# Kernel tuning notes

Measured on AMD Instinct MI355X. Metric: run time of the kernel, lower is better.

Reference implementation:

```python
import jax, jax.numpy as jnp
import numpy as np

NUM_NODES = 100000
NUM_EDGES = 2500000
NUM_GRAPHS = 512
IN_DIM = 14
HID = 32
N_EXTRA_CONVS = 4  # num_layers - 1


def setup_inputs() -> dict:
    key = jax.random.key(0)
    ks = jax.random.split(key, 16)
    x = jax.random.normal(ks[0], (NUM_NODES, IN_DIM), dtype=jnp.float32)
    edge_index = jax.random.randint(ks[1], (2, NUM_EDGES), 0, NUM_NODES, dtype=jnp.int64)
    batch = jnp.sort(jax.random.randint(ks[2], (NUM_NODES,), 0, NUM_GRAPHS, dtype=jnp.int64))
    s = 1.0 / np.sqrt(HID)
    # PyG GraphConv: out = lin_rel(aggr_add(x_j)) + lin_root(x_i); lin_rel has bias, lin_root has no bias
    W_rel1 = jax.random.uniform(ks[3], (IN_DIM, HID), jnp.float32, -s, s)
    b_rel1 = jax.random.uniform(ks[4], (HID,), jnp.float32, -s, s)
    W_root1 = jax.random.uniform(ks[5], (IN_DIM, HID), jnp.float32, -s, s)
    W_rel = jax.random.uniform(ks[6], (N_EXTRA_CONVS, HID, HID), jnp.float32, -s, s)
    b_rel = jax.random.uniform(ks[7], (N_EXTRA_CONVS, HID), jnp.float32, -s, s)
    W_root = jax.random.uniform(ks[8], (N_EXTRA_CONVS, HID, HID), jnp.float32, -s, s)
    lin1_w = jax.random.uniform(ks[9], (HID, HID), jnp.float32, -s, s)
    lin1_b = jax.random.uniform(ks[10], (HID,), jnp.float32, -s, s)
    lin2_w = jax.random.uniform(ks[11], (HID, 2), jnp.float32, -s, s)
    lin2_b = jax.random.uniform(ks[12], (2,), jnp.float32, -s, s)
    return {
        "x": x, "W_rel1": W_rel1, "b_rel1": b_rel1, "W_root1": W_root1,
        "W_rel": W_rel, "b_rel": b_rel, "W_root": W_root,
        "lin1_w": lin1_w, "lin1_b": lin1_b, "lin2_w": lin2_w, "lin2_b": lin2_b,
        "edge_index": edge_index, "batch": batch,
    }


def reference(x, W_rel1, b_rel1, W_root1, W_rel, b_rel, W_root,
              lin1_w, lin1_b, lin2_w, lin2_b, edge_index, batch):
    src, dst = edge_index[0], edge_index[1]

    def graph_conv(h, wr, br, wroot):
        # sum-aggregate neighbor features: scatter-add messages h[src] into dst
        agg = jax.ops.segment_sum(h[src], dst, num_segments=NUM_NODES)
        return agg @ wr + br + h @ wroot

    h = jax.nn.relu(graph_conv(x, W_rel1, b_rel1, W_root1))
    for i in range(N_EXTRA_CONVS):
        h = jax.nn.relu(graph_conv(h, W_rel[i], b_rel[i], W_root[i]))
    # sum pooling per graph
    g = jax.ops.segment_sum(h, batch, num_segments=NUM_GRAPHS)
    g = jax.nn.relu(g @ lin1_w + lin1_b)
    # dropout is identity in eval mode
    logits = g @ lin2_w + lin2_b
    return jax.nn.log_softmax(logits, axis=1)
```

## Files before the change

### kernel.cpp

```cpp
#include <hip/hip_runtime.h>
#include <math.h>

#define N_NODES 100000
#define N_EDGES 2500000
#define N_GRAPHS 512
#define IN_DIM 14
#define HID 32
#define CAP 64

#define BSHIFT 7
#define BNODES 128
#define NB 782
#define NBP 784
#define NBANKS 8
#define SUBCAP 512
#define BCAP 4096
#define CHUNK 4096
#define TB_BIN 512
#define NBLK_E ((N_EDGES + CHUNK - 1) / CHUNK)
#define EPT (CHUNK / TB_BIN)

#define GSTRIDE 8
#define GCUR_N (NBP * NBANKS * GSTRIDE)

typedef unsigned int uint;
typedef unsigned short ushort;
typedef float v2f __attribute__((ext_vector_type(2)));

__device__ inline float bflo(uint w) { return __uint_as_float(w << 16); }
__device__ inline float bfhi(uint w) { return __uint_as_float(w & 0xffff0000u); }
__device__ inline ushort f2bf(float f) {
    uint u = __float_as_uint(f);
    return (ushort)((u + 0x7fffu + ((u >> 16) & 1u)) >> 16);
}

__global__ void bin_edges(const int* __restrict__ src, const int* __restrict__ dst,
                          int* __restrict__ gcur, int* __restrict__ binned) {
    __shared__ int scnt[NBP];
    __shared__ int sbase[NBP];
    int t = threadIdx.x;
    for (int i = t; i < NBP; i += TB_BIN) scnt[i] = 0;
    __syncthreads();
    int base = blockIdx.x * CHUNK;
    int bank = blockIdx.x & (NBANKS - 1);
    int dreg[EPT];
    int rreg[EPT];
#pragma unroll
    for (int j = 0; j < EPT; ++j) {
        int e = base + j * TB_BIN + t;
        dreg[j] = (e < N_EDGES) ? __builtin_nontemporal_load(dst + e) : -1;
        rreg[j] = (dreg[j] >= 0) ? atomicAdd(&scnt[dreg[j] >> BSHIFT], 1) : 0;
    }
    __syncthreads();
    for (int b = t; b < NBP; b += TB_BIN) {
        int c = scnt[b];
        sbase[b] = (c > 0) ? atomicAdd(&gcur[(bank * NBP + b) * GSTRIDE], c) : 0;
    }
    __syncthreads();
#pragma unroll
    for (int j = 0; j < EPT; ++j) {
        int d = dreg[j];
        if (d >= 0) {
            int e = base + j * TB_BIN + t;
            int b = d >> BSHIFT;
            int s = __builtin_nontemporal_load(src + e);
            int pos = sbase[b] + rreg[j];
            if (pos < SUBCAP)
                binned[b * BCAP + bank * SUBCAP + pos] = (s << BSHIFT) | (d & (BNODES - 1));
        }
    }
}

__global__ void build_slots(const int* __restrict__ gcur, const int* __restrict__ binned,
                            int* __restrict__ deg, int* __restrict__ slots) {
    __shared__ int stile[BNODES * CAP];
    __shared__ int sdeg[BNODES];
    int t = threadIdx.x;
    for (int i = t; i < BNODES * CAP; i += 256) stile[i] = N_NODES;
    if (t < BNODES) sdeg[t] = 0;
    __syncthreads();
    int b = blockIdx.x;
#pragma unroll
    for (int k = 0; k < NBANKS; ++k) {
        int cnt = gcur[(k * NBP + b) * GSTRIDE]; if (cnt > SUBCAP) cnt = SUBCAP;
        const int* seg = binned + b * BCAP + k * SUBCAP;
        for (int i = t; i < cnt; i += 256) {
            int w = __builtin_nontemporal_load(seg + i);
            int ld = w & (BNODES - 1), sn = w >> BSHIFT;
            int p = atomicAdd(&sdeg[ld], 1);
            if (p < CAP) stile[ld * CAP + p] = sn;
        }
    }
    __syncthreads();
    int nbase = b * BNODES;
    int rows = N_NODES - nbase; if (rows > BNODES) rows = BNODES;
    int r = t & 127, h = t >> 7;
    if (r < rows) {
        int dv = sdeg[r]; if (dv > CAP) dv = CAP;
        if (h == 0) deg[nbase + r] = dv;
        int n4 = ((dv + 15) >> 4) << 2;
        int4* drow = (int4*)(slots + (size_t)(nbase + r) * CAP);
        const int4* srow = (const int4*)(stile + r * CAP);
        for (int i = h; i < n4; i += 2) drow[i] = srow[i];
    }
}

__global__ void gemm14(const float* __restrict__ h, const float* __restrict__ W,
                       ushort* __restrict__ out, ushort* __restrict__ zrow2,
                       uint2* __restrict__ f0, uint2* __restrict__ f1) {
    __shared__ float sW[IN_DIM][HID];
    int t = threadIdx.x;
    for (int i = t; i < IN_DIM * HID; i += 256) sW[i / HID][i % HID] = W[i];
    if (blockIdx.x == 0) {
        if (t < 4) ((uint4*)(out + (size_t)N_NODES * HID))[t] = make_uint4(0, 0, 0, 0);
        else if (t < 8) ((uint4*)(zrow2 + (size_t)N_NODES * HID))[t - 4] = make_uint4(0, 0, 0, 0);
        else if (t < 12) f0[(size_t)N_NODES * 4 + (t - 8)] = make_uint2(0, 0);
        else if (t < 16) f1[(size_t)N_NODES * 4 + (t - 12)] = make_uint2(0, 0);
    }
    __syncthreads();
    int idx = blockIdx.x * 256 + t;
    if (idx >= N_NODES * HID) return;
    int n = idx >> 5, o = idx & 31;
    const float* hr = h + (long)n * IN_DIM;
    float acc = 0.f;
#pragma unroll
    for (int k = 0; k < IN_DIM; ++k) acc += hr[k] * sW[k][o];
    out[idx] = f2bf(acc);
}

template <bool MUL_REL, int K, bool ROOT_BF16, bool GBF8>
__global__ void conv_fused(const int* __restrict__ deg, const int* __restrict__ slots,
                           const void* __restrict__ gat,
                           const void* __restrict__ root_in,
                           const float* __restrict__ Wrel,
                           const float* __restrict__ bias,
                           const float* __restrict__ Wroot,
                           ushort* __restrict__ outb,
                           uint2* __restrict__ outf8) {
    __shared__ float sWrel[MUL_REL ? HID * HID : 1];
    __shared__ float sWroot[K * HID];
    __shared__ float sb[HID];
    int t = threadIdx.x;
    if (MUL_REL)
        for (int i = t; i < HID * HID; i += 256) sWrel[i] = Wrel[i];
    for (int i = t; i < K * HID; i += 256) sWroot[i] = Wroot[i];
    if (t < HID) sb[t] = bias[t];
    __syncthreads();

    int n = blockIdx.x * 64 + (t >> 2);
    if (n >= N_NODES) return;
    int q = t & 3;

    int dn = __builtin_nontemporal_load(deg + n); if (dn > CAP) dn = CAP;
    int rounds = (dn + 7) >> 3;
    const int* sl = slots + (size_t)n * CAP;
    int2 my[8];
#pragma unroll
    for (int r = 0; r < 8; ++r)
        if (r < rounds) {
            long w = __builtin_nontemporal_load((const long*)(sl + r * 8 + q * 2));
            my[r].x = (int)(w & 0xffffffffL);
            my[r].y = (int)(w >> 32);
        }

    float a[8] = {0.f, 0.f, 0.f, 0.f, 0.f, 0.f, 0.f, 0.f};
#pragma unroll
    for (int r = 0; r < 8; ++r) {
        if (r < rounds) {
#pragma unroll
            for (int j = 0; j < 8; ++j) {
                int c = __shfl((j & 1) ? my[r].y : my[r].x, j >> 1, 4);
                if constexpr (GBF8) {
                    uint2 v = ((const uint2*)gat)[(size_t)c * 4 + q];
                    v2f p0 = __builtin_amdgcn_cvt_pk_f32_bf8(v.x, false);
                    v2f p1 = __builtin_amdgcn_cvt_pk_f32_bf8(v.x, true);
                    v2f p2 = __builtin_amdgcn_cvt_pk_f32_bf8(v.y, false);
                    v2f p3 = __builtin_amdgcn_cvt_pk_f32_bf8(v.y, true);
                    a[0] += p0.x; a[1] += p0.y; a[2] += p1.x; a[3] += p1.y;
                    a[4] += p2.x; a[5] += p2.y; a[6] += p3.x; a[7] += p3.y;
                } else {
                    uint4 v = *(const uint4*)((const ushort*)gat + (size_t)c * HID + q * 8);
                    a[0] += bflo(v.x); a[1] += bfhi(v.x);
                    a[2] += bflo(v.y); a[3] += bfhi(v.y);
                    a[4] += bflo(v.z); a[5] += bfhi(v.z);
                    a[6] += bflo(v.w); a[7] += bfhi(v.w);
                }
            }
        }
    }

    float r8[8];
#pragma unroll
    for (int o = 0; o < 8; ++o) r8[o] = sb[q * 8 + o];

    if constexpr (MUL_REL) {
#pragma unroll
        for (int cl = 0; cl < 4; ++cl) {
#pragma unroll
            for (int j = 0; j < 8; ++j) {
                float av = __shfl(a[j], cl, 4);
                const float* w = &sWrel[(cl * 8 + j) * HID + q * 8];
#pragma unroll
                for (int o = 0; o < 8; ++o) r8[o] += av * w[o];
            }
        }
    } else {
#pragma unroll
        for (int o = 0; o < 8; ++o) r8[o] += a[o];
    }

    if constexpr (ROOT_BF16) {
        uint4 h4 = *(const uint4*)((const ushort*)root_in + (size_t)n * HID + q * 8);
        float hh[8] = {bflo(h4.x), bfhi(h4.x), bflo(h4.y), bfhi(h4.y),
                       bflo(h4.z), bfhi(h4.z), bflo(h4.w), bfhi(h4.w)};
#pragma unroll
        for (int cl = 0; cl < 4; ++cl) {
#pragma unroll
            for (int j = 0; j < 8; ++j) {
                float hv = __shfl(hh[j], cl, 4);
                const float* w = &sWroot[(cl * 8 + j) * HID + q * 8];
#pragma unroll
                for (int o = 0; o < 8; ++o) r8[o] += hv * w[o];
            }
        }
    } else {
        const float* hr = (const float*)root_in + (long)n * K;
#pragma unroll
        for (int k = 0; k < K; ++k) {
            float hv = hr[k];
            const float* w = &sWroot[k * HID + q * 8];
#pragma unroll
            for (int o = 0; o < 8; ++o) r8[o] += hv * w[o];
        }
    }

    float v[8];
#pragma unroll
    for (int o = 0; o < 8; ++o) v[o] = fmaxf(r8[o], 0.f);

    uint pw[4];
#pragma unroll
    for (int m = 0; m < 4; ++m)
        pw[m] = (uint)f2bf(v[2 * m]) | ((uint)f2bf(v[2 * m + 1]) << 16);
    *(uint4*)(outb + (size_t)n * HID + q * 8) = make_uint4(pw[0], pw[1], pw[2], pw[3]);

    uint w0 = __builtin_amdgcn_cvt_pk_bf8_f32(v[0], v[1], 0u, false);
    w0 = __builtin_amdgcn_cvt_pk_bf8_f32(v[2], v[3], w0, true);
    uint w1 = __builtin_amdgcn_cvt_pk_bf8_f32(v[4], v[5], 0u, false);
    w1 = __builtin_amdgcn_cvt_pk_bf8_f32(v[6], v[7], w1, true);
    outf8[(size_t)n * 4 + q] = make_uint2(w0, w1);
}

__global__ __launch_bounds__(256) void pool_head(
        const ushort* __restrict__ h, const int* __restrict__ batch,
        const float* __restrict__ w1, const float* __restrict__ b1,
        const float* __restrict__ w2, const float* __restrict__ b2,
        float* __restrict__ out) {
    __shared__ float sW1[HID][HID];
    __shared__ float sb1[HID];
    __shared__ float sW2[HID][2];
    __shared__ float sacc[8][HID];
    __shared__ float sg[HID];
    __shared__ float sl[2][HID];
    int t = threadIdx.x;
    int gid = blockIdx.x;
    for (int i = t; i < HID * HID; i += 256) sW1[i / HID][i % HID] = w1[i];
    if (t < HID) sb1[t] = b1[t];
    if (t < HID * 2) sW2[t >> 1][t & 1] = w2[t];

    int lo = 0, hi = N_NODES;
    while (lo < hi) { int m = (lo + hi) >> 1; if (batch[m] < gid) lo = m + 1; else hi = m; }
    int s = lo;
    hi = N_NODES;
    while (lo < hi) { int m = (lo + hi) >> 1; if (batch[m] < gid + 1) lo = m + 1; else hi = m; }
    int e = lo;

    int f = t & 31, r = t >> 5;
    float acc = 0.f;
    for (int n = s + r; n < e; n += 8)
        acc += bflo((uint)h[(size_t)n * HID + f]);
    sacc[r][f] = acc;
    __syncthreads();
    if (t < HID) {
        float gv = 0.f;
#pragma unroll
        for (int rr = 0; rr < 8; ++rr) gv += sacc[rr][t];
        sg[t] = gv;
    }
    __syncthreads();
    if (t < HID) {
        float a = sb1[t];
#pragma unroll
        for (int k = 0; k < HID; ++k) a += sg[k] * sW1[k][t];
        a = fmaxf(a, 0.f);
        sl[0][t] = a * sW2[t][0];
        sl[1][t] = a * sW2[t][1];
    }
    __syncthreads();
    if (t == 0) {
        float l0 = b2[0], l1 = b2[1];
#pragma unroll
        for (int o = 0; o < HID; ++o) { l0 += sl[0][o]; l1 += sl[1][o]; }
        float m = fmaxf(l0, l1);
        float lse = m + logf(expf(l0 - m) + expf(l1 - m));
        out[gid * 2 + 0] = l0 - lse;
        out[gid * 2 + 1] = l1 - lse;
    }
}

extern "C" void kernel_launch(void* const* d_in, const int* in_sizes, int n_in,
                              void* d_out, int out_size, void* d_ws, size_t ws_size,
                              hipStream_t stream) {
    const float* x      = (const float*)d_in[0];
    const float* W_rel1 = (const float*)d_in[1];
    const float* b_rel1 = (const float*)d_in[2];
    const float* W_root1= (const float*)d_in[3];
    const float* W_rel  = (const float*)d_in[4];
    const float* b_rel  = (const float*)d_in[5];
    const float* W_root = (const float*)d_in[6];
    const float* lin1_w = (const float*)d_in[7];
    const float* lin1_b = (const float*)d_in[8];
    const float* lin2_w = (const float*)d_in[9];
    const float* lin2_b = (const float*)d_in[10];
    const int*   ei     = (const int*)d_in[11];
    const int*   batch  = (const int*)d_in[12];
    float* out = (float*)d_out;

    const int* src = ei;
    const int* dst = ei + N_EDGES;

    int*    gcur   = (int*)d_ws;
    int*    binned = gcur + GCUR_N;
    int*    deg    = binned + NB * BCAP;
    int*    slots  = deg + N_NODES + 32;
    ushort* B0b    = (ushort*)(slots + (size_t)N_NODES * CAP);
    ushort* B1b    = B0b + (size_t)(N_NODES + 1) * HID;
    uint2*  F0     = (uint2*)(B1b + (size_t)(N_NODES + 1) * HID);
    uint2*  F1     = F0 + (size_t)(N_NODES + 1) * 4;

    dim3 blk(256);
    dim3 grd_no((N_NODES * HID + 255) / 256);
    dim3 grd_cv((N_NODES + 63) / 64);

    hipMemsetAsync(gcur, 0, GCUR_N * sizeof(int), stream);
    bin_edges<<<dim3(NBLK_E), dim3(TB_BIN), 0, stream>>>(src, dst, gcur, binned);
    build_slots<<<dim3(NB), blk, 0, stream>>>(gcur, binned, deg, slots);

    gemm14<<<grd_no, blk, 0, stream>>>(x, W_rel1, B0b, B1b, F0, F1);
    conv_fused<false, IN_DIM, false, false><<<grd_cv, blk, 0, stream>>>(
        deg, slots, (const void*)B0b, (const void*)x, nullptr, b_rel1, W_root1, B1b, F1);

    ushort* cur = B1b;  uint2* curf = F1;
    ushort* nxt = B0b;  uint2* nxtf = F0;
    for (int i = 0; i < 4; ++i) {
        conv_fused<true, HID, true, true><<<grd_cv, blk, 0, stream>>>(
            deg, slots, (const void*)curf, (const void*)cur, W_rel + i * HID * HID,
            b_rel + i * HID, W_root + i * HID * HID, nxt, nxtf);
        ushort* ts = cur; cur = nxt; nxt = ts;
        uint2*  tf = curf; curf = nxtf; nxtf = tf;
    }

    pool_head<<<dim3(N_GRAPHS), blk, 0, stream>>>(cur, batch, lin1_w, lin1_b,
                                                  lin2_w, lin2_b, out);
}
```

Baseline: 324.5 us.

## Aggregate raw padded bf16 input before first-layer transform instead of pre-multiplying

The first conv layer previously ran a 14x32 GEMM over every node to produce a 32-wide bf16 table and then gathered those 64-byte rows per edge. Now x is padded to 16 bf16 values per node (32-byte rows), neighbours are gathered and summed in that narrow space, and W_rel and W_root are applied afterwards inside one fused kernel. This halves the per-edge gather bytes and drops the separate GEMM pass. The cost is an extra padding kernel, and the input is rounded to bf16 before aggregation, which changes precision slightly.

Result: faster. 311.9 us (-3.9%).

```diff
diff --git a/kernel.cpp b/kernel.cpp
--- a/kernel.cpp
+++ b/kernel.cpp
@@ -105,27 +105,112 @@
     }
 }
 
-__global__ void gemm14(const float* __restrict__ h, const float* __restrict__ W,
-                       ushort* __restrict__ out, ushort* __restrict__ zrow2,
-                       uint2* __restrict__ f0, uint2* __restrict__ f1) {
-    __shared__ float sW[IN_DIM][HID];
-    int t = threadIdx.x;
-    for (int i = t; i < IN_DIM * HID; i += 256) sW[i / HID][i % HID] = W[i];
+__global__ void pad_x(const float* __restrict__ x, ushort* __restrict__ x16,
+                      uint2* __restrict__ f0, uint2* __restrict__ f1) {
+    int t = threadIdx.x;
     if (blockIdx.x == 0) {
-        if (t < 4) ((uint4*)(out + (size_t)N_NODES * HID))[t] = make_uint4(0, 0, 0, 0);
-        else if (t < 8) ((uint4*)(zrow2 + (size_t)N_NODES * HID))[t - 4] = make_uint4(0, 0, 0, 0);
-        else if (t < 12) f0[(size_t)N_NODES * 4 + (t - 8)] = make_uint2(0, 0);
-        else if (t < 16) f1[(size_t)N_NODES * 4 + (t - 12)] = make_uint2(0, 0);
-    }
-    __syncthreads();
+        if (t < 2) ((uint4*)(x16 + (size_t)N_NODES * 16))[t] = make_uint4(0, 0, 0, 0);
+        else if (t < 6) f0[(size_t)N_NODES * 4 + (t - 2)] = make_uint2(0, 0);
+        else if (t < 10) f1[(size_t)N_NODES * 4 + (t - 6)] = make_uint2(0, 0);
+    }
     int idx = blockIdx.x * 256 + t;
-    if (idx >= N_NODES * HID) return;
-    int n = idx >> 5, o = idx & 31;
-    const float* hr = h + (long)n * IN_DIM;
-    float acc = 0.f;
-#pragma unroll
-    for (int k = 0; k < IN_DIM; ++k) acc += hr[k] * sW[k][o];
-    out[idx] = f2bf(acc);
+    if (idx >= N_NODES * 16) return;
+    int n = idx >> 4, k = idx & 15;
+    x16[idx] = (k < IN_DIM) ? f2bf(x[(size_t)n * IN_DIM + k]) : (ushort)0;
+}
+
+__global__ void conv1_fused(const int* __restrict__ deg, const int* __restrict__ slots,
+                            const ushort* __restrict__ x16,
+                            const float* __restrict__ Wrel,
+                            const float* __restrict__ bias,
+                            const float* __restrict__ Wroot,
+                            ushort* __restrict__ outb,
+                            uint2* __restrict__ outf8) {
+    __shared__ float sWrel[16 * HID];
+    __shared__ float sWroot[16 * HID];
+    __shared__ float sb[HID];
+    int t = threadIdx.x;
+    for (int i = t; i < 16 * HID; i += 256) {
+        sWrel[i]  = (i < IN_DIM * HID) ? Wrel[i] : 0.f;
+        sWroot[i] = (i < IN_DIM * HID) ? Wroot[i] : 0.f;
+    }
+    if (t < HID) sb[t] = bias[t];
+    __syncthreads();
+
+    int n = blockIdx.x * 64 + (t >> 2);
+    if (n >= N_NODES) return;
+    int q = t & 3;
+
+    int dn = __builtin_nontemporal_load(deg + n); if (dn > CAP) dn = CAP;
+    int rounds = (dn + 7) >> 3;
+    const int* sl = slots + (size_t)n * CAP;
+    int2 my[8];
+#pragma unroll
+    for (int r = 0; r < 8; ++r)
+        if (r < rounds) {
+            long w = __builtin_nontemporal_load((const long*)(sl + r * 8 + q * 2));
+            my[r].x = (int)(w & 0xffffffffL);
+            my[r].y = (int)(w >> 32);
+        }
+
+    v2f a2[2] = {{0.f, 0.f}, {0.f, 0.f}};
+#pragma unroll
+    for (int r = 0; r < 8; ++r) {
+        if (r < rounds) {
+#pragma unroll
+            for (int j = 0; j < 8; ++j) {
+                int c = __shfl((j & 1) ? my[r].y : my[r].x, j >> 1, 4);
+                uint2 v = *(const uint2*)(x16 + (size_t)c * 16 + q * 4);
+                a2[0] += (v2f){bflo(v.x), bfhi(v.x)};
+                a2[1] += (v2f){bflo(v.y), bfhi(v.y)};
+            }
+        }
+    }
+    float a[4] = {a2[0].x, a2[0].y, a2[1].x, a2[1].y};
+
+    float r8[8];
+#pragma unroll
+    for (int o = 0; o < 8; ++o) r8[o] = sb[q * 8 + o];
+
+#pragma unroll
+    for (int cl = 0; cl < 4; ++cl) {
+#pragma unroll
+        for (int j = 0; j < 4; ++j) {
+            float av = __shfl(a[j], cl, 4);
+            const float* w = &sWrel[(cl * 4 + j) * HID + q * 8];
+#pragma unroll
+            for (int o = 0; o < 8; ++o) r8[o] += av * w[o];
+        }
+    }
+
+    uint2 h2 = *(const uint2*)(x16 + (size_t)n * 16 + q * 4);
+    float hh[4] = {bflo(h2.x), bfhi(h2.x), bflo(h2.y), bfhi(h2.y)};
+#pragma unroll
+    for (int cl = 0; cl < 4; ++cl) {
+#pragma unroll
+        for (int j = 0; j < 4; ++j) {
+            float hv = __shfl(hh[j], cl, 4);
+            const float* w = &sWroot[(cl * 4 + j) * HID + q * 8];
+#pragma unroll
+            for (int o = 0; o < 8; ++o) r8[o] += hv * w[o];
+        }
+    }
+
+    float v[8];
+#pragma unroll
+    for (int o = 0; o < 8; ++o) v[o] = fmaxf(r8[o], 0.f);
+
+    uint pw[4];
+#pragma unroll
+    for (int m = 0; m < 4; ++m)
+        pw[m] = (uint)f2bf(v[2 * m]) | ((uint)f2bf(v[2 * m + 1]) << 16);
+    *(uint4*)(outb + (size_t)n * HID + q * 8) = make_uint4(pw[0], pw[1], pw[2], pw[3]);
+
+    uint w0 = __builtin_amdgcn_cvt_pk_bf8_f32(v[0], v[1], 0u, false);
+    w0 = __builtin_amdgcn_cvt_pk_bf8_f32(v[2], v[3], w0, true);
+    uint w1 = __builtin_amdgcn_cvt_pk_bf8_f32(v[4], v[5], 0u, false);
+    w1 = __builtin_amdgcn_cvt_pk_bf8_f32(v[6], v[7], w1, true);
+    outf8[(size_t)n * 4 + q] = make_uint2(w0, w1);
 }
 
 template <bool MUL_REL, int K, bool ROOT_BF16, bool GBF8>
@@ -337,18 +422,19 @@
     ushort* B1b    = B0b + (size_t)(N_NODES + 1) * HID;
     uint2*  F0     = (uint2*)(B1b + (size_t)(N_NODES + 1) * HID);
     uint2*  F1     = F0 + (size_t)(N_NODES + 1) * 4;
+    ushort* X16    = (ushort*)(F1 + (size_t)(N_NODES + 1) * 4);
 
     dim3 blk(256);
-    dim3 grd_no((N_NODES * HID + 255) / 256);
+    dim3 grd_px((N_NODES * 16 + 255) / 256);
     dim3 grd_cv((N_NODES + 63) / 64);
 
     hipMemsetAsync(gcur, 0, GCUR_N * sizeof(int), stream);
     bin_edges<<<dim3(NBLK_E), dim3(TB_BIN), 0, stream>>>(src, dst, gcur, binned);
+    pad_x<<<grd_px, blk, 0, stream>>>(x, X16, F0, F1);
     build_slots<<<dim3(NB), blk, 0, stream>>>(gcur, binned, deg, slots);
 
-    gemm14<<<grd_no, blk, 0, stream>>>(x, W_rel1, B0b, B1b, F0, F1);
-    conv_fused<false, IN_DIM, false, false><<<grd_cv, blk, 0, stream>>>(
-        deg, slots, (const void*)B0b, (const void*)x, nullptr, b_rel1, W_root1, B1b, F1);
+    conv1_fused<<<grd_cv, blk, 0, stream>>>(deg, slots, X16, W_rel1, b_rel1,
+                                            W_root1, B1b, F1);
 
     ushort* cur = B1b;  uint2* curf = F1;
     ushort* nxt = B0b;  uint2* nxtf = F0;
```
